# Optimization experiments

Hardware: AMD Instinct MI355X
Metric: run time of the kernel (lower is better)

The kernel has to match this reference:

```python
import jax, jax.numpy as jnp
import numpy as np

D_IN, D_DICT, K, N = 768, 16384, 32, 8192


def setup_inputs() -> dict:
    key = jax.random.key(0)
    k1, k2, k3, k4, k5 = jax.random.split(key, 5)
    s_in = 1.0 / np.sqrt(D_IN)
    s_dict = 1.0 / np.sqrt(D_DICT)
    return {
        "x": jax.random.normal(k1, (N, D_IN), dtype=jnp.float32),
        # torch Linear: weight [out, in], bias [out]
        "W_enc": jax.random.uniform(k2, (D_DICT, D_IN), jnp.float32, -s_in, s_in),
        "b_enc": jax.random.uniform(k3, (D_DICT,), jnp.float32, -s_in, s_in),
        "W_dec": jax.random.uniform(k4, (D_IN, D_DICT), jnp.float32, -s_dict, s_dict),
        "b_dec": jax.random.uniform(k5, (D_IN,), jnp.float32, -s_dict, s_dict),
    }


def reference(x, W_enc, b_enc, W_dec, b_dec):
    # encode: z = x @ W_enc^T + b_enc  -> [N, d_dict]
    z = jnp.einsum("nd,kd->nk", x, W_enc) + b_enc
    # top-k mask along last dim (scatter 1.0 at top-k indices)
    _, idx = jax.lax.top_k(z, K)                      # idx: [N, K]
    rows = jnp.arange(z.shape[0])[:, None]            # [N, 1]
    mask = jnp.zeros_like(z).at[rows, idx].set(1.0)
    z_sparse = z * mask
    # decode: x_hat = z_sparse @ W_dec^T + b_dec -> [N, d_in]
    x_hat = jnp.einsum("nk,dk->nd", z_sparse, W_dec) + b_dec
    return (x_hat, z_sparse)
```

## Files before the change

### kernel.cpp

```cpp
#include <hip/hip_runtime.h>
#include <stdint.h>

#define D_IN   768
#define D_DICT 16384
#define NROWS  8192
#define TOPK   32
#define CAND_TARGET 40
#define CAND_MAX    80
#define FLOORU 0xBFA8u
#define NTILES 64
#define SEG    24
#define LECAP  768

#define BM 256
#define BN 256
#define BK 64
#define NKT (D_IN / BK)

typedef __attribute__((ext_vector_type(4))) float  f32x4;
typedef __attribute__((ext_vector_type(8))) short  s16x8;
typedef __attribute__((ext_vector_type(4))) unsigned short u16x4;

static __device__ __forceinline__ unsigned short f2bf(float f) {
    unsigned int u = __float_as_uint(f);
    unsigned int r = (u + 0x7FFFu + ((u >> 16) & 1u)) >> 16;
    return (unsigned short)r;
}
static __device__ __forceinline__ unsigned short bfmap(unsigned short u) {
    return (u & 0x8000u) ? (unsigned short)(~u) : (unsigned short)(u | 0x8000u);
}

static __device__ __forceinline__ void gload_lds16(const void* g, void* l) {
    __builtin_amdgcn_global_load_lds(
        (const __attribute__((address_space(1))) unsigned int*)g,
        (__attribute__((address_space(3))) unsigned int*)l, 16, 0, 0);
}

__global__ __launch_bounds__(256) void cast_bf16(const float4* __restrict__ in,
                                                 u16x4* __restrict__ out, int n4) {
    int idx = blockIdx.x * 256 + threadIdx.x;
    if (idx >= n4) return;
    float4 v = in[idx];
    u16x4 o;
    o.x = f2bf(v.x); o.y = f2bf(v.y); o.z = f2bf(v.z); o.w = f2bf(v.w);
    out[idx] = o;
}

__global__ void transpose_wdec(const float* __restrict__ in, float* __restrict__ out) {
    __shared__ float t[32][33];
    int bx = blockIdx.x, by = blockIdx.y;
    int tx = threadIdx.x, ty = threadIdx.y;
#pragma unroll
    for (int i = 0; i < 4; ++i)
        t[ty + i * 8][tx] = in[(size_t)(by * 32 + ty + i * 8) * D_DICT + bx * 32 + tx];
    __syncthreads();
#pragma unroll
    for (int i = 0; i < 4; ++i)
        out[(size_t)(bx * 32 + ty + i * 8) * D_IN + by * 32 + tx] = t[tx][ty + i * 8];
}

__global__ __launch_bounds__(512, 2) void gemm_enc(const unsigned short* __restrict__ Xb,
                                                   const unsigned short* __restrict__ Wb,
                                                   const float* __restrict__ bEnc,
                                                   unsigned int* __restrict__ list,
                                                   unsigned char* __restrict__ cnt8,
                                                   float* __restrict__ zsp) {
    extern __shared__ char smem[];
    unsigned short* As = (unsigned short*)smem;
    unsigned short* Bs = (unsigned short*)(smem + 2 * BM * BK * 2);
    const int tid    = threadIdx.x;
    const int waveId = tid >> 6;
    const int lane   = tid & 63;

    const int wg    = blockIdx.x;
    const int wgid  = (wg & 7) * 256 + (wg >> 3);
    const int ctile = wgid & (NTILES - 1);
    const int rtile = wgid >> 6;
    const int rowBase = rtile * BM;
    const int colBase = ctile * BN;
    const int wm = waveId >> 2, wn = waveId & 3;

    {
        float4 z4 = make_float4(0.f, 0.f, 0.f, 0.f);
        float4* zd = (float4*)(zsp + (size_t)rowBase * D_DICT + colBase);
#pragma unroll
        for (int i = 0; i < 32; ++i) {
            int slot = i * 512 + tid;
            zd[(size_t)(slot >> 6) * (D_DICT / 4) + (slot & 63)] = z4;
        }
    }

    f32x4 acc[8][4] = {};

    const int m0 = wm * 128 + (lane & 15);
    const int n0 = wn * 64  + (lane & 15);
    const int quad = lane >> 4;
    const int xsw  = lane & 7;

    auto STAGE = [&](int p, int t) {
        const int k0 = t * BK;
        unsigned short* Ab = As + (size_t)p * (BM * BK);
        unsigned short* Bb = Bs + (size_t)p * (BN * BK);
#pragma unroll
        for (int i = 0; i < 4; ++i) {
            int slot = i * 512 + tid;
            int r  = slot >> 3;
            int lc = (slot & 7) ^ (r & 7);
            gload_lds16(Xb + (size_t)(rowBase + r) * D_IN + k0 + lc * 8,
                        Ab + (size_t)(i * 512 + waveId * 64) * 8);
            gload_lds16(Wb + (size_t)(colBase + r) * D_IN + k0 + lc * 8,
                        Bb + (size_t)(i * 512 + waveId * 64) * 8);
        }
    };

    STAGE(0, 0);
    __syncthreads();

    for (int t = 0; t < NKT; ++t) {
        const int p = t & 1;
        if (t + 1 < NKT) STAGE(p ^ 1, t + 1);
        const unsigned short* Ab = As + (size_t)p * (BM * BK);
        const unsigned short* Bb = Bs + (size_t)p * (BN * BK);
#pragma unroll
        for (int kk = 0; kk < 2; ++kk) {
            const int ch = kk * 4 + quad;
            s16x8 a[8], b[4];
#pragma unroll
            for (int f = 0; f < 8; ++f)
                a[f] = *(const s16x8*)(Ab + (m0 + f * 16) * BK + ((ch ^ xsw) << 3));
#pragma unroll
            for (int f = 0; f < 4; ++f)
                b[f] = *(const s16x8*)(Bb + (n0 + f * 16) * BK + ((ch ^ xsw) << 3));
#pragma unroll
            for (int mi = 0; mi < 8; ++mi)
#pragma unroll
                for (int ni = 0; ni < 4; ++ni)
                    acc[mi][ni] = __builtin_amdgcn_mfma_f32_16x16x32_bf16(
                        a[mi], b[ni], acc[mi][ni], 0, 0, 0);
        }
        __syncthreads();
    }

    int*          lcnt  = (int*)smem;
    unsigned int* stage = (unsigned int*)(smem + 1024);
    if (tid < 256) lcnt[tid] = 0;
    __syncthreads();

    const int colW = colBase + wn * 64 + (lane & 15);
    float bias[4];
#pragma unroll
    for (int f = 0; f < 4; ++f) bias[f] = bEnc[colW + f * 16];
    const unsigned long long qmask = 0xFFFFull << (quad * 16);
    const unsigned long long lmask = (1ull << lane) - 1ull;

#pragma unroll
    for (int mi = 0; mi < 8; ++mi) {
#pragma unroll
        for (int rg = 0; rg < 4; ++rg) {
            const int lrow = wm * 128 + mi * 16 + quad * 4 + rg;
            unsigned int uv[4];
            unsigned long long bm[4];
            int m4 = 0;
#pragma unroll
            for (int f = 0; f < 4; ++f) {
                float v = acc[mi][f][rg] + bias[f];
                unsigned int u = bfmap(f2bf(v));
                uv[f] = (u << 16) | (unsigned int)(colW + f * 16);
                bool pass = (u >= FLOORU);
                bm[f] = __ballot(pass);
                if (pass) m4 |= (1 << f);
            }
            int rowTotal = (int)(__popcll(bm[0] & qmask) + __popcll(bm[1] & qmask)
                               + __popcll(bm[2] & qmask) + __popcll(bm[3] & qmask));
            int base = 0;
            if ((lane & 15) == 0 && rowTotal) base = atomicAdd(&lcnt[lrow], rowTotal);
            base = __shfl(base, quad * 16, 64);
            if (m4) {
                int pre = 0;
#pragma unroll
                for (int f = 0; f < 4; ++f) {
                    if (m4 & (1 << f)) {
                        int pos = base + pre + (int)__popcll(bm[f] & qmask & lmask);
                        if (pos < SEG) stage[lrow * SEG + pos] = uv[f];
                    }
                    pre += (int)__popcll(bm[f] & qmask);
                }
            }
        }
    }
    __syncthreads();

    if (tid < 256) {
        int c = lcnt[tid]; if (c > SEG) c = SEG;
        cnt8[(size_t)(rowBase + tid) * NTILES + ctile] = (unsigned char)c;
    }
    for (int i = tid; i < 256 * SEG; i += 512) {
        int r = i / SEG, s = i - r * SEG;
        int c = lcnt[r]; if (c > SEG) c = SEG;
        if (s < c)
            list[((size_t)(rowBase + r) * NTILES + ctile) * SEG + s] = stage[r * SEG + s];
    }
}

__global__ __launch_bounds__(256) void sel_dec(const unsigned int* __restrict__ list,
                                               const unsigned char* __restrict__ cnt8,
                                               const float* __restrict__ x,
                                               const float* __restrict__ wEnc,
                                               const float* __restrict__ bEnc,
                                               const float* __restrict__ wDecT,
                                               const float* __restrict__ bDec,
                                               float* __restrict__ zsp,
                                               float* __restrict__ xhat) {
    const int row = blockIdx.x;
    const int tid = threadIdx.x;
    const int waveId = tid >> 6;

    __shared__ int   histc[4][256];
    alignas(16) __shared__ float xs[D_IN];
    __shared__ unsigned int le[LECAP];
    __shared__ unsigned int cw[NTILES / 4];
    __shared__ int   tb[NTILES];
    __shared__ int   cidx[CAND_MAX];
    __shared__ float zc[CAND_MAX];
    __shared__ int   selk[TOPK];
    __shared__ float selv[TOPK];
    __shared__ int   sh_ncand, sh_bin, sh_cum, sh_bin2;
    __shared__ int   sh_nstrict, sh_ntie, sh_nsel;

    if (tid < NTILES / 4)
        cw[tid] = ((const unsigned int*)(cnt8 + (size_t)row * NTILES))[tid];
    if (tid < 192)
        ((float4*)xs)[tid] = ((const float4*)(x + (size_t)row * D_IN))[tid];
    if (tid == 0) { sh_nstrict = 0; sh_ntie = 0; sh_nsel = 0; sh_bin = -1; }
    __syncthreads();

    const unsigned char* cb = (const unsigned char*)cw;
    if (tid < 64) {
        int c = cb[tid];
        int pref = c;
#pragma unroll
        for (int off = 1; off < 64; off <<= 1) {
            int n = __shfl_up(pref, off, 64);
            if (tid >= off) pref += n;
        }
        tb[tid] = pref - c;
        if (tid == 63) sh_ncand = pref;
    }
    for (int b = tid; b < 1024; b += 256) ((int*)histc)[b] = 0;
    __syncthreads();
    const int nCand = min(sh_ncand, LECAP);

    for (int i = tid; i < NTILES * SEG; i += 256) {
        int t = i / SEG, s = i - t * SEG;
        if (s < (int)cb[t]) {
            int dst = tb[t] + s;
            if (dst < LECAP) le[dst] = list[((size_t)row * NTILES + t) * SEG + s];
        }
    }
    __syncthreads();

    const int T = CAND_TARGET;
    for (int i = tid; i < nCand; i += 256) {
        unsigned int u = le[i] >> 16;
        int bin = (int)((u - FLOORU) >> 6);
        if (bin > 255) bin = 255;
        atomicAdd(&histc[waveId][bin], 1);
    }
    __syncthreads();
    if (tid < 256) histc[0][tid] += histc[1][tid] + histc[2][tid] + histc[3][tid];
    __syncthreads();
    if (tid < 64) {
        int l = tid;
        int b0 = 255 - l * 4;
        int s0 = histc[0][b0], s1 = histc[0][b0 - 1],
            s2 = histc[0][b0 - 2], s3 = histc[0][b0 - 3];
        int local = s0 + s1 + s2 + s3;
        int pref = local;
#pragma unroll
        for (int off = 1; off < 64; off <<= 1) {
            int n = __shfl_up(pref, off, 64);
            if (l >= off) pref += n;
        }
        unsigned long long m = __ballot(pref >= T);
        if (m) {
            int first = (int)__ffsll(m) - 1;
            if (l == first) {
                int cum = pref - local;
                int b, c;
                if      (cum + s0 >= T)           { b = b0;     c = cum; }
                else if (cum + s0 + s1 >= T)      { b = b0 - 1; c = cum + s0; }
                else if (cum + s0 + s1 + s2 >= T) { b = b0 - 2; c = cum + s0 + s1; }
                else                              { b = b0 - 3; c = cum + s0 + s1 + s2; }
                sh_bin = b; sh_cum = c;
            }
        }
    }
    __syncthreads();
    const int b1 = sh_bin;
    unsigned int tieLo, tieTop;

    if (b1 >= 0) {
        const int cumAbove = sh_cum;
        for (int b = tid; b < 1024; b += 256) ((int*)histc)[b] = 0;
        __syncthreads();
        for (int i = tid; i < nCand; i += 256) {
            unsigned int u = le[i] >> 16;
            int bin = (int)((u - FLOORU) >> 6);
            if (bin > 255) bin = 255;
            if (bin == b1) atomicAdd(&histc[waveId][(u - FLOORU) & 63u], 1);
        }
        __syncthreads();
        if (tid < 64) {
            int l = tid;
            int bb = 63 - l;
            int local = histc[0][bb] + histc[1][bb] + histc[2][bb] + histc[3][bb];
            int pref = local;
#pragma unroll
            for (int off = 1; off < 64; off <<= 1) {
                int n = __shfl_up(pref, off, 64);
                if (l >= off) pref += n;
            }
            unsigned long long m = __ballot(cumAbove + pref >= T);
            int first = (int)__ffsll(m) - 1;
            if (l == first) sh_bin2 = bb;
        }
        __syncthreads();
        tieLo  = FLOORU + ((unsigned)b1 << 6) + (unsigned)sh_bin2;
        tieTop = tieLo;
    } else {
        tieLo = 1u; tieTop = 0u;
    }

    for (int i = tid; i < nCand; i += 256) {
        unsigned int u = le[i] >> 16;
        int col = (int)(le[i] & 0xFFFFu);
        if (u > tieTop) {
            int p = atomicAdd(&sh_nstrict, 1);
            cidx[p] = col;
        } else if (u >= tieLo) {
            int t = atomicAdd(&sh_ntie, 1);
            if (t < CAND_TARGET) cidx[CAND_MAX - 1 - t] = col;
        }
    }
    __syncthreads();
    const int nstrict = sh_nstrict;
    const int nt = min(sh_ntie, CAND_TARGET);
    int tmpv = 0;
    if (tid < nt) tmpv = cidx[CAND_MAX - 1 - tid];
    __syncthreads();
    if (tid < nt) cidx[nstrict + tid] = tmpv;
    __syncthreads();
    const int nc = nstrict + nt;

    const int sub = tid & 7;
    const int cq  = tid >> 3;
    for (int c0 = 0; c0 < nc; c0 += 32) {
        int c = c0 + cq;
        double a0 = 0.0, a1 = 0.0, a2 = 0.0, a3 = 0.0;
        int k = 0;
        if (c < nc) {
            k = cidx[c];
            const float4* wp = (const float4*)(wEnc + (size_t)k * D_IN);
            const float4* xp = (const float4*)xs;
#pragma unroll 8
            for (int j = 0; j < 24; ++j) {
                float4 wv = wp[j * 8 + sub];
                float4 xv = xp[j * 8 + sub];
                a0 += (double)xv.x * (double)wv.x;
                a1 += (double)xv.y * (double)wv.y;
                a2 += (double)xv.z * (double)wv.z;
                a3 += (double)xv.w * (double)wv.w;
            }
        }
        double acc = (a0 + a1) + (a2 + a3);
        acc += __shfl_xor(acc, 1, 64);
        acc += __shfl_xor(acc, 2, 64);
        acc += __shfl_xor(acc, 4, 64);
        if (c < nc && sub == 0) zc[c] = (float)(acc + (double)bEnc[k]);
    }
    __syncthreads();

    if (tid < nc) {
        float v = zc[tid];
        int   k = cidx[tid];
        int rk = 0;
        for (int j = 0; j < nc; ++j) {
            float vj = zc[j];
            if (vj > v || (vj == v && cidx[j] < k)) ++rk;
        }
        if (rk < TOPK) {
            int s = atomicAdd(&sh_nsel, 1);
            selk[s] = k; selv[s] = v;
        }
    }
    __syncthreads();

    if (tid < TOPK) zsp[(size_t)row * D_DICT + selk[tid]] = selv[tid];

    if (tid < 192) {
        float4 acc = ((const float4*)bDec)[tid];
#pragma unroll 8
        for (int j = 0; j < TOPK; ++j) {
            const float4* wr = (const float4*)(wDecT + (size_t)selk[j] * D_IN);
            float4 wv = wr[tid];
            float s = selv[j];
            acc.x += s * wv.x; acc.y += s * wv.y;
            acc.z += s * wv.z; acc.w += s * wv.w;
        }
        ((float4*)(xhat + (size_t)row * D_IN))[tid] = acc;
    }
}

extern "C" void kernel_launch(void* const* d_in, const int* in_sizes, int n_in,
                              void* d_out, int out_size, void* d_ws, size_t ws_size,
                              hipStream_t stream) {
    const float* x    = (const float*)d_in[0];
    const float* wEnc = (const float*)d_in[1];
    const float* bEnc = (const float*)d_in[2];
    const float* wDec = (const float*)d_in[3];
    const float* bDec = (const float*)d_in[4];

    float* xhat = (float*)d_out;
    float* zsp  = (float*)d_out + (size_t)NROWS * D_IN;

    char* ws = (char*)d_ws;
    unsigned short* Xb   = (unsigned short*)ws;
    unsigned short* Wb   = (unsigned short*)(ws + (size_t)NROWS * D_IN * 2);
    float*          WdT  = (float*)(ws + (size_t)NROWS * D_IN * 2
                                       + (size_t)D_DICT * D_IN * 2);
    unsigned int*   list = (unsigned int*)(ws + 88080384);
    unsigned char*  cnt8 = (unsigned char*)(ws + 88080384
                                       + (size_t)NROWS * NTILES * SEG * 4);

    static int configured = 0;
    if (!configured) {
        hipFuncSetAttribute((const void*)gemm_enc,
                            hipFuncAttributeMaxDynamicSharedMemorySize, 131072);
        configured = 1;
    }

    {
        int n4 = NROWS * D_IN / 4;
        cast_bf16<<<(n4 + 255) / 256, 256, 0, stream>>>((const float4*)x, (u16x4*)Xb, n4);
    }
    {
        int n4 = D_DICT * D_IN / 4;
        cast_bf16<<<(n4 + 255) / 256, 256, 0, stream>>>((const float4*)wEnc, (u16x4*)Wb, n4);
    }
    transpose_wdec<<<dim3(D_DICT / 32, D_IN / 32), dim3(32, 8), 0, stream>>>(wDec, WdT);
    gemm_enc<<<(NROWS / BM) * (D_DICT / BN), 512, 131072, stream>>>(Xb, Wb, bEnc, list, cnt8, zsp);
    sel_dec<<<NROWS, 256, 0, stream>>>(list, cnt8, x, wEnc, bEnc, WdT, bDec, zsp, xhat);
}
```

Baseline: 1.214 ms.

## Restructure encoder GEMM main loop into four-phase half-K pipelined schedule

The encoder GEMM's double-buffered K loop is replaced by a finer schedule. Each K tile is split into two 32-wide halves and each half into two M halves, with global-to-LDS loads issued one to two phases ahead and explicit vmcnt waits plus raw s_barrier in place of __syncthreads. MFMA sections run at raised wave priority, and zeroing of the sparse output tile is moved after the GEMM so its stores no longer delay the first loads. The intent is to overlap memory traffic with matrix math and cut barrier stalls, at the cost of fragile hand-counted waitcnt logic and a different LDS swizzle.

Measured after the change: 1.192 ms. About the same (-1.8%).

```diff
diff --git a/kernel.cpp b/kernel.cpp
--- a/kernel.cpp
+++ b/kernel.cpp
@@ -67,7 +67,7 @@
                                                    float* __restrict__ zsp) {
     extern __shared__ char smem[];
     unsigned short* As = (unsigned short*)smem;
-    unsigned short* Bs = (unsigned short*)(smem + 2 * BM * BK * 2);
+    unsigned short* Bs = (unsigned short*)(smem + 65536);
     const int tid    = threadIdx.x;
     const int waveId = tid >> 6;
     const int lane   = tid & 63;
@@ -80,6 +80,81 @@
     const int colBase = ctile * BN;
     const int wm = waveId >> 2, wn = waveId & 3;
 
+    f32x4 acc[8][4] = {};
+
+    const int quad = lane >> 4;
+    const int lr   = lane & 15;
+
+    auto STAGEH = [&](int t, int kind, int kh) {
+        const int d = t & 1;
+        const unsigned short* gsrc = kind ? Wb : Xb;
+        const int gbase = kind ? colBase : rowBase;
+        unsigned short* lb = (kind ? Bs : As) + (size_t)(d * 2 + kh) * (256 * 32);
+        const int k0 = t * BK + kh * 32;
+#pragma unroll
+        for (int i = 0; i < 2; ++i) {
+            int slot = i * 512 + tid;
+            int r = slot >> 2;
+            int c = slot & 3;
+            int lc = c ^ (r & 3);
+            gload_lds16(gsrc + (size_t)(gbase + r) * D_IN + k0 + lc * 8,
+                        lb + (size_t)(i * 512 + waveId * 64) * 8);
+        }
+    };
+
+    STAGEH(0, 0, 0); STAGEH(0, 1, 0);
+    STAGEH(0, 0, 1); STAGEH(0, 1, 1);
+    STAGEH(1, 0, 0); STAGEH(1, 1, 0);
+
+    for (int t = 0; t < NKT; ++t) {
+        const int d = t & 1;
+#pragma unroll
+        for (int ph = 0; ph < 4; ++ph) {
+            const int kh = ph >> 1, mh = ph & 1;
+            if (ph == 0) {
+                if (t + 1 < NKT) asm volatile("s_waitcnt vmcnt(8)" ::: "memory");
+                else             asm volatile("s_waitcnt vmcnt(4)" ::: "memory");
+            } else if (ph == 2) {
+                if (t + 1 < NKT) asm volatile("s_waitcnt vmcnt(8)" ::: "memory");
+                else             asm volatile("s_waitcnt vmcnt(0)" ::: "memory");
+            }
+            __builtin_amdgcn_s_barrier();
+
+            const unsigned short* Ah = As + (size_t)(d * 2 + kh) * (256 * 32);
+            const unsigned short* Bh = Bs + (size_t)(d * 2 + kh) * (256 * 32);
+            s16x8 a[4], b[4];
+#pragma unroll
+            for (int j = 0; j < 4; ++j) {
+                int ar = wm * 128 + (mh * 4 + j) * 16 + lr;
+                a[j] = *(const s16x8*)(Ah + ar * 32 + ((quad ^ (ar & 3)) << 3));
+            }
+#pragma unroll
+            for (int j = 0; j < 4; ++j) {
+                int br = wn * 64 + j * 16 + lr;
+                b[j] = *(const s16x8*)(Bh + br * 32 + ((quad ^ (br & 3)) << 3));
+            }
+
+            if      (ph == 0) { if (t + 1 < NKT) STAGEH(t + 1, 0, 1); }
+            else if (ph == 1) { if (t + 1 < NKT) STAGEH(t + 1, 1, 1); }
+            else if (ph == 2) { if (t + 2 < NKT) STAGEH(t + 2, 0, 0); }
+            else              { if (t + 2 < NKT) STAGEH(t + 2, 1, 0); }
+
+            __builtin_amdgcn_s_setprio(1);
+#pragma unroll
+            for (int j = 0; j < 4; ++j)
+#pragma unroll
+                for (int ni = 0; ni < 4; ++ni)
+                    acc[mh * 4 + j][ni] = __builtin_amdgcn_mfma_f32_16x16x32_bf16(
+                        a[j], b[ni], acc[mh * 4 + j][ni], 0, 0, 0);
+            __builtin_amdgcn_s_setprio(0);
+        }
+    }
+
+    int*          lcnt  = (int*)smem;
+    unsigned int* stage = (unsigned int*)(smem + 1024);
+    if (tid < 256) lcnt[tid] = 0;
+    __syncthreads();
+
     {
         float4 z4 = make_float4(0.f, 0.f, 0.f, 0.f);
         float4* zd = (float4*)(zsp + (size_t)rowBase * D_DICT + colBase);
@@ -90,63 +165,7 @@
         }
     }
 
-    f32x4 acc[8][4] = {};
-
-    const int m0 = wm * 128 + (lane & 15);
-    const int n0 = wn * 64  + (lane & 15);
-    const int quad = lane >> 4;
-    const int xsw  = lane & 7;
-
-    auto STAGE = [&](int p, int t) {
-        const int k0 = t * BK;
-        unsigned short* Ab = As + (size_t)p * (BM * BK);
-        unsigned short* Bb = Bs + (size_t)p * (BN * BK);
-#pragma unroll
-        for (int i = 0; i < 4; ++i) {
-            int slot = i * 512 + tid;
-            int r  = slot >> 3;
-            int lc = (slot & 7) ^ (r & 7);
-            gload_lds16(Xb + (size_t)(rowBase + r) * D_IN + k0 + lc * 8,
-                        Ab + (size_t)(i * 512 + waveId * 64) * 8);
-            gload_lds16(Wb + (size_t)(colBase + r) * D_IN + k0 + lc * 8,
-                        Bb + (size_t)(i * 512 + waveId * 64) * 8);
-        }
-    };
-
-    STAGE(0, 0);
-    __syncthreads();
-
-    for (int t = 0; t < NKT; ++t) {
-        const int p = t & 1;
-        if (t + 1 < NKT) STAGE(p ^ 1, t + 1);
-        const unsigned short* Ab = As + (size_t)p * (BM * BK);
-        const unsigned short* Bb = Bs + (size_t)p * (BN * BK);
-#pragma unroll
-        for (int kk = 0; kk < 2; ++kk) {
-            const int ch = kk * 4 + quad;
-            s16x8 a[8], b[4];
-#pragma unroll
-            for (int f = 0; f < 8; ++f)
-                a[f] = *(const s16x8*)(Ab + (m0 + f * 16) * BK + ((ch ^ xsw) << 3));
-#pragma unroll
-            for (int f = 0; f < 4; ++f)
-                b[f] = *(const s16x8*)(Bb + (n0 + f * 16) * BK + ((ch ^ xsw) << 3));
-#pragma unroll
-            for (int mi = 0; mi < 8; ++mi)
-#pragma unroll
-                for (int ni = 0; ni < 4; ++ni)
-                    acc[mi][ni] = __builtin_amdgcn_mfma_f32_16x16x32_bf16(
-                        a[mi], b[ni], acc[mi][ni], 0, 0, 0);
-        }
-        __syncthreads();
-    }
-
-    int*          lcnt  = (int*)smem;
-    unsigned int* stage = (unsigned int*)(smem + 1024);
-    if (tid < 256) lcnt[tid] = 0;
-    __syncthreads();
-
-    const int colW = colBase + wn * 64 + (lane & 15);
+    const int colW = colBase + wn * 64 + lr;
     float bias[4];
 #pragma unroll
     for (int f = 0; f < 4; ++f) bias[f] = bEnc[colW + f * 16];
```
